# Performance work log

Hardware: AMD Instinct MI355X
Metric: run time of the kernel (lower is better)

## Reference

```python
import jax, jax.numpy as jnp
import numpy as np

# ---- constant kernels (kornia canny defaults) ----

def _gauss_kernel1d(ksize=5, sigma=1.0):
    x = np.arange(ksize, dtype=np.float32) - (ksize - 1) / 2.0
    g = np.exp(-(x ** 2) / (2.0 * sigma ** 2))
    return (g / g.sum()).astype(np.float32)

_GK = _gauss_kernel1d()
_SOBEL_X = np.array([[-1, 0, 1], [-2, 0, 2], [-1, 0, 1]], np.float32) / 8.0  # normalized=True
_SOBEL_Y = _SOBEL_X.T.copy()

# 8 directional NMS kernels: +1 at center, -1 at neighbor d*45 degrees (kornia order)
_NMS = np.zeros((8, 1, 3, 3), np.float32)
_OFFS = [(0, 1), (1, 1), (1, 0), (1, -1), (0, -1), (-1, -1), (-1, 0), (-1, 1)]
for _i, (_dy, _dx) in enumerate(_OFFS):
    _NMS[_i, 0, 1, 1] = 1.0
    _NMS[_i, 0, 1 + _dy, 1 + _dx] = -1.0


def _conv(x, k):
    return jax.lax.conv_general_dilated(
        x, k, (1, 1), 'VALID', dimension_numbers=('NCHW', 'OIHW', 'NCHW'))


def _canny_dilate(x):
    # x: [B,3,H,W] BGR in [0,1]
    x = x[:, ::-1]  # bgr -> rgb
    gray = 0.299 * x[:, 0:1] + 0.587 * x[:, 1:2] + 0.114 * x[:, 2:3]  # [B,1,H,W]

    # gaussian blur 5x5, sigma=1, reflect padding (separable)
    p = jnp.pad(gray, ((0, 0), (0, 0), (2, 2), (2, 2)), mode='reflect')
    kh = jnp.asarray(_GK).reshape(1, 1, 1, 5)
    kv = jnp.asarray(_GK).reshape(1, 1, 5, 1)
    blurred = _conv(_conv(p, kh), kv)

    # sobel gradients, replicate padding
    sp = jnp.pad(blurred, ((0, 0), (0, 0), (1, 1), (1, 1)), mode='edge')
    sob = jnp.asarray(np.stack([_SOBEL_X, _SOBEL_Y])[:, None])  # (2,1,3,3)
    g = _conv(sp, sob)
    gx, gy = g[:, 0:1], g[:, 1:2]

    mag = jnp.sqrt(gx * gx + gy * gy + 1e-6)  # [B,1,H,W]
    ang45 = jnp.round(jnp.arctan2(gy, gx) * (180.0 / np.pi) / 45.0)  # multiples of 45 deg
    pos_idx = jnp.mod(ang45, 8).astype(jnp.int32)
    neg_idx = jnp.mod(ang45 + 4, 8).astype(jnp.int32)

    # direction-dependent non-maximum suppression
    nms = _conv(jnp.pad(mag, ((0, 0), (0, 0), (1, 1), (1, 1))), jnp.asarray(_NMS))  # [B,8,H,W]
    pos = jnp.take_along_axis(nms, pos_idx, axis=1)
    neg = jnp.take_along_axis(nms, neg_idx, axis=1)
    is_max = jnp.minimum(pos, neg) > 0.0
    mag = mag * is_max

    # morphological dilation, 5x5 ones kernel, geodesic border (pad with -max_val)
    MAX_VAL = 1e4
    padded = jnp.pad(mag, ((0, 0), (0, 0), (2, 2), (2, 2)), constant_values=-MAX_VAL)
    out = jax.lax.reduce_window(padded, -jnp.inf, jax.lax.max,
                                (1, 1, 5, 5), (1, 1, 1, 1), 'VALID')
    return out


def setup_inputs() -> dict:
    key = jax.random.key(0)
    x = jax.random.uniform(key, (32, 3, 512, 512), dtype=jnp.float32)
    return {'x': x}


def reference(x):
    return _canny_dilate(x)
```

## Files before the change

### kernel.cpp

```cpp
#include <hip/hip_runtime.h>
#include <math.h>

#define IMW 512
#define SEG 32
#define NSEG (512/SEG)
#define NSTRIP 10
#define OUTW 52

__device__ __forceinline__ int reflect512(int i) {
    int a = i < 0 ? -i : i;
    int b = 1022 - a;
    return a < b ? a : b;
}
__device__ __forceinline__ float bperm(int a4, float v) {
    return __int_as_float(__builtin_amdgcn_ds_bpermute(a4, __float_as_int(v)));
}

__global__ __launch_bounds__(256)
void canny_pipe(const float* __restrict__ x, float* __restrict__ out) {
    const int lane  = threadIdx.x & 63;
    const int unit  = blockIdx.x * 4 + (threadIdx.x >> 6);
    const int img   = unit / (NSTRIP * NSEG);
    const int rem   = unit - img * (NSTRIP * NSEG);
    const int strip = rem / NSEG;
    const int seg   = rem - strip * NSEG;
    const int Y0 = seg * SEG, Y1 = Y0 + SEG;
    const int x0 = strip * OUTW - 6;
    const int xv = x0 + lane;
    const int xr = reflect512(xv);
    const bool inimg  = (xv >= 0) && (xv < IMW);
    const bool stlane = (lane >= 6) && (lane < 58) && (xv < IMW);
    const int l4  = lane << 2;
    const int aL4 = (min(max(xv - 1, 0), 511) - x0) << 2;
    const int aR4 = (min(max(xv + 1, 0), 511) - x0) << 2;

    const float* base = x + (size_t)img * 3 * IMW * IMW;
    const float* c0p = base + (size_t)0 * IMW * IMW + xr;
    const float* c1p = base + (size_t)1 * IMW * IMW + xr;
    const float* c2p = base + (size_t)2 * IMW * IMW + xr;
    float* outp = out + (size_t)img * IMW * IMW + xv;

    const float K0 = 0.054488684549643f, K1 = 0.244201342003233f, K2 = 0.402619946931554f;

    float hb0=0,hb1=0,hb2=0,hb3=0,hb4=0;
    float hx0=0,hx1=0,hx2=0, hy0=0,hy1=0,hy2=0;
    float mg0=0,mg1=0,mg2=0;
    int   ax0=0, ax1=0;
    float cm0=0,cm1=0,cm2=0,cm3=0,cm4=0;

    int r0 = reflect512(Y0 - 6);
    float p0 = c0p[(size_t)r0 * IMW];
    float p1 = c1p[(size_t)r0 * IMW];
    float p2 = c2p[(size_t)r0 * IMW];

    for (int v = Y0 - 6; v <= Y1 + 5; ++v) {
        float gray = 0.299f * p2 + 0.587f * p1 + 0.114f * p0;
        int rn = reflect512(v + 1);
        p0 = c0p[(size_t)rn * IMW];
        p1 = c1p[(size_t)rn * IMW];
        p2 = c2p[(size_t)rn * IMW];

        float gl1 = bperm(l4 - 4, gray), gl2 = bperm(l4 - 8, gray);
        float gr1 = bperm(l4 + 4, gray), gr2 = bperm(l4 + 8, gray);
        hb0 = hb1; hb1 = hb2; hb2 = hb3; hb3 = hb4;
        hb4 = K0 * (gl2 + gr2) + K1 * (gl1 + gr1) + K2 * gray;

        float blur = K0 * (hb0 + hb4) + K1 * (hb1 + hb3) + K2 * hb2;
        float bl = bperm(aL4, blur), br = bperm(aR4, blur);
        hx0 = hx1; hx1 = hx2; hx2 = br - bl;
        hy0 = hy1; hy1 = hy2; hy2 = bl + 2.f * blur + br;

        int g = v - 3;
        float hxa = (g == 0)   ? hx1 : hx0;
        float hxc = (g == 511) ? hx1 : hx2;
        float hya = (g == 0)   ? hy1 : hy0;
        float hyc = (g == 511) ? hy1 : hy2;
        float gxv = (hxa + 2.f * hx1 + hxc) * 0.125f;
        float gyv = (hyc - hya) * 0.125f;
        float mag = sqrtf(gxv * gxv + gyv * gyv + 1e-6f);
        float axm = fabsf(gxv), aym = fabsf(gyv);
        int axis;
        if (aym <= 0.41421356237309515f * axm)      axis = 0;
        else if (aym >= 2.4142135623730951f * axm)  axis = 2;
        else axis = ((gxv >= 0.f) == (gyv >= 0.f)) ? 1 : 3;
        mg0 = mg1; mg1 = mg2; mg2 = inimg ? mag : 0.f;
        ax0 = ax1; ax1 = axis;

        int m = v - 4;
        float magm = (m == 0)   ? 0.f : mg0;
        float magc = mg1;
        float magp = (m == 511) ? 0.f : mg2;
        float gcp = bperm(l4 + 4, magc), gcm = bperm(l4 - 4, magc);
        float gpp = bperm(l4 + 4, magp), gpm = bperm(l4 - 4, magp);
        float gmm = bperm(l4 - 4, magm), gmp = bperm(l4 + 4, magm);
        int d = ax0;
        float mp = (d == 0) ? gcp : (d == 1) ? gpp : (d == 2) ? magp : gpm;
        float mn = (d == 0) ? gcm : (d == 1) ? gmm : (d == 2) ? magm : gmp;
        float msk = (inimg && fminf(magc - mp, magc - mn) > 0.f) ? magc : 0.f;

        float s1 = fmaxf(bperm(l4 - 4, msk), bperm(l4 + 4, msk));
        float s2 = fmaxf(bperm(l4 - 8, msk), bperm(l4 + 8, msk));
        cm0 = cm1; cm1 = cm2; cm2 = cm3; cm3 = cm4;
        cm4 = fmaxf(fmaxf(s1, s2), msk);

        int y = v - 6;
        if (y >= Y0) {
            float c0 = (y >= 2)   ? cm0 : 0.f;
            float c1 = (y >= 1)   ? cm1 : 0.f;
            float c3 = (y <= 510) ? cm3 : 0.f;
            float c4 = (y <= 509) ? cm4 : 0.f;
            float val = fmaxf(fmaxf(fmaxf(c0, c1), fmaxf(cm2, c3)), c4);
            if (stlane) outp[(size_t)y * IMW] = val;
        }
    }
}

extern "C" void kernel_launch(void* const* d_in, const int* in_sizes, int n_in,
                              void* d_out, int out_size, void* d_ws, size_t ws_size,
                              hipStream_t stream) {
    const float* x = (const float*)d_in[0];
    float* out = (float*)d_out;
    const int units = 32 * NSTRIP * NSEG;
    dim3 grid(units / 4);
    canny_pipe<<<grid, 256, 0, stream>>>(x, out);
}
```

Measured before the change: 175.1 us.

## Specialize interior segments without border checks and unroll ring-buffer pipeline

Splits the row pipeline into a templated interior path with no reflect or border predicates and an edge path that keeps them. The shift-register variables become ring buffers indexed by t%5 under unroll-5, so the register shuffles disappear. Segment height drops from 32 to 23 rows, which gives more work units (23 segments of 23 rows, 529 rows, with the last segment guarded by y<512). Shorter segments mean the 12-row halo recompute is a larger share of the work, and that could offset the savings from removing the branches.

```diff
diff --git a/kernel.cpp b/kernel.cpp
--- a/kernel.cpp
+++ b/kernel.cpp
@@ -2,10 +2,11 @@
 #include <math.h>
 
 #define IMW 512
-#define SEG 32
-#define NSEG (512/SEG)
+#define SEG 23
+#define NSEG 23
 #define NSTRIP 10
 #define OUTW 52
+#define TRIPS (SEG + 12)
 
 __device__ __forceinline__ int reflect512(int i) {
     int a = i < 0 ? -i : i;
@@ -16,6 +17,111 @@
     return __int_as_float(__builtin_amdgcn_ds_bpermute(a4, __float_as_int(v)));
 }
 
+template<bool EDGE>
+__device__ __forceinline__ void pipe_run(
+    const float* __restrict__ base0, const float* __restrict__ base1,
+    const float* __restrict__ base2, float* __restrict__ outp,
+    int Y0, int xr, bool inimg, bool stlane, int l4, int aL4, int aR4)
+{
+    const float K0 = 0.054488684549643f, K1 = 0.244201342003233f, K2 = 0.402619946931554f;
+
+    float hb[5], hx[5], hy[5], mg[5], cm[5];
+    int   ax[5];
+    #pragma unroll
+    for (int i = 0; i < 5; ++i) { hb[i]=0.f; hx[i]=0.f; hy[i]=0.f; mg[i]=0.f; cm[i]=0.f; ax[i]=0; }
+
+    int r0i = Y0 - 6;
+    if (EDGE) r0i = reflect512(r0i);
+    float p0 = (base0 + (size_t)r0i * IMW)[xr];
+    float p1 = (base1 + (size_t)r0i * IMW)[xr];
+    float p2 = (base2 + (size_t)r0i * IMW)[xr];
+
+    #pragma unroll 5
+    for (int t = 0; t < TRIPS; ++t) {
+        const int v = Y0 - 6 + t;
+
+        float gray = 0.299f * p2 + 0.587f * p1 + 0.114f * p0;
+        int rn = v + 1;
+        if (EDGE) rn = reflect512(rn);
+        const float* r0 = base0 + (size_t)rn * IMW;
+        const float* r1 = base1 + (size_t)rn * IMW;
+        const float* r2 = base2 + (size_t)rn * IMW;
+        p0 = r0[xr]; p1 = r1[xr]; p2 = r2[xr];
+
+        float gl1 = bperm(l4 - 4, gray), gl2 = bperm(l4 - 8, gray);
+        float gr1 = bperm(l4 + 4, gray), gr2 = bperm(l4 + 8, gray);
+        hb[t % 5] = K0 * (gl2 + gr2) + K1 * (gl1 + gr1) + K2 * gray;
+
+        float blur = K0 * (hb[(t + 1) % 5] + hb[t % 5])
+                   + K1 * (hb[(t + 2) % 5] + hb[(t + 4) % 5])
+                   + K2 * hb[(t + 3) % 5];
+
+        float bl = bperm(aL4, blur), br = bperm(aR4, blur);
+        hx[t % 5] = br - bl;
+        hy[t % 5] = bl + 2.f * blur + br;
+
+        float hxa, hxc, hya, hyc;
+        if (EDGE) {
+            const int g = v - 3;
+            hxa = (g == 0)   ? hx[(t + 4) % 5] : hx[(t + 3) % 5];
+            hya = (g == 0)   ? hy[(t + 4) % 5] : hy[(t + 3) % 5];
+            hxc = (g == 511) ? hx[(t + 4) % 5] : hx[t % 5];
+            hyc = (g == 511) ? hy[(t + 4) % 5] : hy[t % 5];
+        } else {
+            hxa = hx[(t + 3) % 5]; hya = hy[(t + 3) % 5];
+            hxc = hx[t % 5];       hyc = hy[t % 5];
+        }
+        float gxv = (hxa + 2.f * hx[(t + 4) % 5] + hxc) * 0.125f;
+        float gyv = (hyc - hya) * 0.125f;
+        float mag = sqrtf(gxv * gxv + gyv * gyv + 1e-6f);
+        float axm = fabsf(gxv), aym = fabsf(gyv);
+        int axis;
+        if (aym <= 0.41421356237309515f * axm)      axis = 0;
+        else if (aym >= 2.4142135623730951f * axm)  axis = 2;
+        else axis = ((gxv >= 0.f) == (gyv >= 0.f)) ? 1 : 3;
+        mg[t % 5] = inimg ? mag : 0.f;
+        ax[t % 5] = axis;
+
+        const int m = v - 4;
+        float magc = mg[(t + 4) % 5];
+        float magp, magm;
+        if (EDGE) {
+            magp = (m >= 511) ? 0.f : mg[t % 5];
+            magm = (m <= 0)   ? 0.f : mg[(t + 3) % 5];
+        } else {
+            magp = mg[t % 5];
+            magm = mg[(t + 3) % 5];
+        }
+        float gcp = bperm(l4 + 4, magc), gcm = bperm(l4 - 4, magc);
+        float gpp = bperm(l4 + 4, magp), gpm = bperm(l4 - 4, magp);
+        float gmm = bperm(l4 - 4, magm), gmp = bperm(l4 + 4, magm);
+        int d = ax[(t + 4) % 5];
+        float mp = (d == 0) ? gcp : (d == 1) ? gpp : (d == 2) ? magp : gpm;
+        float mn = (d == 0) ? gcm : (d == 1) ? gmm : (d == 2) ? magm : gmp;
+        bool keep = fminf(magc - mp, magc - mn) > 0.f;
+        if (EDGE) keep = keep && (m >= 0) && (m <= 511);
+        float msk = keep ? magc : 0.f;
+
+        float s1 = fmaxf(bperm(l4 - 4, msk), bperm(l4 + 4, msk));
+        float s2 = fmaxf(bperm(l4 - 8, msk), bperm(l4 + 8, msk));
+        cm[t % 5] = fmaxf(fmaxf(s1, s2), msk);
+
+        if (t >= 12) {
+            const int y = v - 6;
+            float c0 = cm[(t + 1) % 5], c1 = cm[(t + 2) % 5];
+            float c2 = cm[(t + 3) % 5];
+            float c3 = cm[(t + 4) % 5], c4 = cm[t % 5];
+            if (EDGE) {
+                if (y < 2)   { c0 = 0.f; if (y < 1)   c1 = 0.f; }
+                if (y > 509) { c4 = 0.f; if (y > 510) c3 = 0.f; }
+            }
+            float val = fmaxf(fmaxf(fmaxf(c0, c1), fmaxf(c2, c3)), c4);
+            if ((!EDGE || y < 512) && stlane)
+                outp[(size_t)y * IMW] = val;
+        }
+    }
+}
+
 __global__ __launch_bounds__(256)
 void canny_pipe(const float* __restrict__ x, float* __restrict__ out) {
     const int lane  = threadIdx.x & 63;
@@ -24,7 +130,7 @@
     const int rem   = unit - img * (NSTRIP * NSEG);
     const int strip = rem / NSEG;
     const int seg   = rem - strip * NSEG;
-    const int Y0 = seg * SEG, Y1 = Y0 + SEG;
+    const int Y0 = seg * SEG;
     const int x0 = strip * OUTW - 6;
     const int xv = x0 + lane;
     const int xr = reflect512(xv);
@@ -35,84 +141,15 @@
     const int aR4 = (min(max(xv + 1, 0), 511) - x0) << 2;
 
     const float* base = x + (size_t)img * 3 * IMW * IMW;
-    const float* c0p = base + (size_t)0 * IMW * IMW + xr;
-    const float* c1p = base + (size_t)1 * IMW * IMW + xr;
-    const float* c2p = base + (size_t)2 * IMW * IMW + xr;
+    const float* b0 = base;
+    const float* b1 = base + (size_t)IMW * IMW;
+    const float* b2 = base + (size_t)2 * IMW * IMW;
     float* outp = out + (size_t)img * IMW * IMW + xv;
 
-    const float K0 = 0.054488684549643f, K1 = 0.244201342003233f, K2 = 0.402619946931554f;
-
-    float hb0=0,hb1=0,hb2=0,hb3=0,hb4=0;
-    float hx0=0,hx1=0,hx2=0, hy0=0,hy1=0,hy2=0;
-    float mg0=0,mg1=0,mg2=0;
-    int   ax0=0, ax1=0;
-    float cm0=0,cm1=0,cm2=0,cm3=0,cm4=0;
-
-    int r0 = reflect512(Y0 - 6);
-    float p0 = c0p[(size_t)r0 * IMW];
-    float p1 = c1p[(size_t)r0 * IMW];
-    float p2 = c2p[(size_t)r0 * IMW];
-
-    for (int v = Y0 - 6; v <= Y1 + 5; ++v) {
-        float gray = 0.299f * p2 + 0.587f * p1 + 0.114f * p0;
-        int rn = reflect512(v + 1);
-        p0 = c0p[(size_t)rn * IMW];
-        p1 = c1p[(size_t)rn * IMW];
-        p2 = c2p[(size_t)rn * IMW];
-
-        float gl1 = bperm(l4 - 4, gray), gl2 = bperm(l4 - 8, gray);
-        float gr1 = bperm(l4 + 4, gray), gr2 = bperm(l4 + 8, gray);
-        hb0 = hb1; hb1 = hb2; hb2 = hb3; hb3 = hb4;
-        hb4 = K0 * (gl2 + gr2) + K1 * (gl1 + gr1) + K2 * gray;
-
-        float blur = K0 * (hb0 + hb4) + K1 * (hb1 + hb3) + K2 * hb2;
-        float bl = bperm(aL4, blur), br = bperm(aR4, blur);
-        hx0 = hx1; hx1 = hx2; hx2 = br - bl;
-        hy0 = hy1; hy1 = hy2; hy2 = bl + 2.f * blur + br;
-
-        int g = v - 3;
-        float hxa = (g == 0)   ? hx1 : hx0;
-        float hxc = (g == 511) ? hx1 : hx2;
-        float hya = (g == 0)   ? hy1 : hy0;
-        float hyc = (g == 511) ? hy1 : hy2;
-        float gxv = (hxa + 2.f * hx1 + hxc) * 0.125f;
-        float gyv = (hyc - hya) * 0.125f;
-        float mag = sqrtf(gxv * gxv + gyv * gyv + 1e-6f);
-        float axm = fabsf(gxv), aym = fabsf(gyv);
-        int axis;
-        if (aym <= 0.41421356237309515f * axm)      axis = 0;
-        else if (aym >= 2.4142135623730951f * axm)  axis = 2;
-        else axis = ((gxv >= 0.f) == (gyv >= 0.f)) ? 1 : 3;
-        mg0 = mg1; mg1 = mg2; mg2 = inimg ? mag : 0.f;
-        ax0 = ax1; ax1 = axis;
-
-        int m = v - 4;
-        float magm = (m == 0)   ? 0.f : mg0;
-        float magc = mg1;
-        float magp = (m == 511) ? 0.f : mg2;
-        float gcp = bperm(l4 + 4, magc), gcm = bperm(l4 - 4, magc);
-        float gpp = bperm(l4 + 4, magp), gpm = bperm(l4 - 4, magp);
-        float gmm = bperm(l4 - 4, magm), gmp = bperm(l4 + 4, magm);
-        int d = ax0;
-        float mp = (d == 0) ? gcp : (d == 1) ? gpp : (d == 2) ? magp : gpm;
-        float mn = (d == 0) ? gcm : (d == 1) ? gmm : (d == 2) ? magm : gmp;
-        float msk = (inimg && fminf(magc - mp, magc - mn) > 0.f) ? magc : 0.f;
-
-        float s1 = fmaxf(bperm(l4 - 4, msk), bperm(l4 + 4, msk));
-        float s2 = fmaxf(bperm(l4 - 8, msk), bperm(l4 + 8, msk));
-        cm0 = cm1; cm1 = cm2; cm2 = cm3; cm3 = cm4;
-        cm4 = fmaxf(fmaxf(s1, s2), msk);
-
-        int y = v - 6;
-        if (y >= Y0) {
-            float c0 = (y >= 2)   ? cm0 : 0.f;
-            float c1 = (y >= 1)   ? cm1 : 0.f;
-            float c3 = (y <= 510) ? cm3 : 0.f;
-            float c4 = (y <= 509) ? cm4 : 0.f;
-            float val = fmaxf(fmaxf(fmaxf(c0, c1), fmaxf(cm2, c3)), c4);
-            if (stlane) outp[(size_t)y * IMW] = val;
-        }
-    }
+    if (seg >= 1 && seg <= 20)
+        pipe_run<false>(b0, b1, b2, outp, Y0, xr, inimg, stlane, l4, aL4, aR4);
+    else
+        pipe_run<true >(b0, b1, b2, outp, Y0, xr, inimg, stlane, l4, aL4, aR4);
 }
 
 extern "C" void kernel_launch(void* const* d_in, const int* in_sizes, int n_in,
```

Measured after the change: 181.9 us. 1.04x slower.
